# Optimization experiments

Hardware: AMD Instinct MI355X
Metric: run time of the kernel (lower is better)

## Reference

```python
import jax, jax.numpy as jnp
import numpy as np

B, C, H, W = 8, 4, 64, 2048
KH, KW = 3, 5
PH, PW = KH // 2, KW // 2
NUM_ITERS = 3
THETA_GAMMA = 0.9
THETA_ALPHA = 0.9
THETA_BETA = 0.015


def smoothness_kernel(theta):
    # Gaussian over squared window offsets, center zeroed, placed on class diagonal
    hs = jnp.arange(KH, dtype=jnp.float32) - KH // 2
    ws = jnp.arange(KW, dtype=jnp.float32) - KW // 2
    pdist = hs[:, None] ** 2 + ws[None, :] ** 2  # (KH,KW)
    k = jnp.exp(-pdist / (2.0 * theta ** 2))
    k = k.at[KH // 2, KW // 2].set(0.0)
    kernel = jnp.zeros((C, C, KH, KW), jnp.float32)
    kernel = kernel.at[jnp.arange(C), jnp.arange(C)].set(k)
    return kernel


def unfold_neighbors(x):
    # x: (b, c, H, W) -> (b, c, KH*KW-1, H*W), center tap excluded; row-major (kh,kw)
    b, c = x.shape[0], x.shape[1]
    xp = jnp.pad(x, ((0, 0), (0, 0), (PH, PH), (PW, PW)))
    taps = [xp[:, :, dh:dh + H, dw:dw + W]
            for dh in range(KH) for dw in range(KW)]
    K = KH * KW
    del taps[K // 2]  # exclude center pixel
    patches = jnp.stack(taps, axis=2)  # (b, c, K-1, H, W)
    return patches.reshape(b, c, K - 1, H * W)


def conv_same(x, kernel):
    return jax.lax.conv_general_dilated(
        x, kernel, window_strides=(1, 1), padding=[(PH, PH), (PW, PW)],
        dimension_numbers=('NCHW', 'OIHW', 'NCHW'))


def setup_inputs() -> dict:
    key = jax.random.key(0)
    k1, k2, k3 = jax.random.split(key, 3)
    unary = jax.random.normal(k1, (B, C, H, W), jnp.float32)
    xyz = jax.random.normal(k2, (B, 3, H, W), jnp.float32)
    mask = (jax.random.uniform(k3, (B, H, W)) > 0.1).astype(jnp.float32)
    weight_appearance = jnp.ones((1, C, 1, 1), jnp.float32) * 0.1
    weight_smoothness = jnp.ones((1, C, 1, 1), jnp.float32) * 0.02
    compat_w = 1.0 - jnp.eye(C, dtype=jnp.float32)  # Potts label compatibility (O,I)
    return {
        'unary': unary, 'xyz': xyz, 'mask': mask,
        'weight_appearance': weight_appearance,
        'weight_smoothness': weight_smoothness,
        'compat_w': compat_w,
    }


def reference(unary, xyz, mask, weight_appearance, weight_smoothness, compat_w):
    kernel_gamma = smoothness_kernel(THETA_GAMMA)
    kernel_alpha = smoothness_kernel(THETA_ALPHA)
    theta_beta = jnp.full((C,), THETA_BETA, jnp.float32)

    # precompute appearance (bilateral) kernel from xyz; detached in the original
    anchor = xyz.reshape(B, 3, 1, H * W)
    nb = unfold_neighbors(xyz)  # (B,3,14,HW)
    pdist = ((nb - anchor) ** 2).sum(axis=1, keepdims=True)  # (B,1,14,HW)
    kernel_beta = jnp.exp(-pdist / (2.0 * theta_beta[None, :, None, None] ** 2))  # (B,C,14,HW)
    kernel_beta = jax.lax.stop_gradient(kernel_beta)

    m = mask[:, None]  # (B,1,H,W)
    Q = unary
    for _ in range(NUM_ITERS):
        Q = jax.nn.softmax(Q, axis=1)
        k_smooth = conv_same(Q, kernel_gamma)
        # appearance message passing: masked windowed gather weighted by kernel_beta
        masked_Q = Q * m
        Q_nb = unfold_neighbors(masked_Q)  # (B,C,14,HW)
        exp_app = (Q_nb * kernel_beta).sum(axis=2).reshape(B, C, H, W) * m
        exp_smooth = conv_same(Q, kernel_alpha)
        k_app = exp_app * exp_smooth
        weighted_k = weight_smoothness * k_smooth + weight_appearance * k_app
        pairwise = jnp.einsum('oc,bchw->bohw', compat_w, weighted_k)
        Q = unary - pairwise
    return Q
```

## Files before the change

kernel.cpp:

```cpp
#include <hip/hip_runtime.h>
#include <hip/hip_fp16.h>

#define Bsz 8
#define Cn  4
#define Hn  64
#define Wn  2048
#define HW  (Hn*Wn)
#define NPIX (Bsz*HW)

#define PW     2052
#define PROWS  66
#define PBATCH (PW*PROWS)
#define PTOT   (Bsz*PBATCH)

#define G1 0.53940824f
#define G2 0.29096127f
#define G4 0.08465836f
#define G5 0.04566536f

struct Half4 { __half2 lo, hi; };
struct Half8 { __half2 h[4]; };

__device__ __forceinline__ __half2 bcast_lo(__half2 v) { return __half2half2(__low2half(v)); }
__device__ __forceinline__ __half2 bcast_hi(__half2 v) { return __half2half2(__high2half(v)); }

__global__ __launch_bounds__(256) void crf_prep(const float* __restrict__ unary,
                                                const float* __restrict__ xyz,
                                                const float* __restrict__ mask,
                                                Half8* __restrict__ BA,
                                                Half8* __restrict__ BB,
                                                Half4* __restrict__ S0,
                                                Half4* __restrict__ S1) {
    int c = blockIdx.x * 256 + threadIdx.x;
    if (c >= PTOT) return;
    int b  = c / PBATCH;
    int rr = c - b * PBATCH;
    int r  = rr / PW;
    int w  = rr - r * PW;
    int hp = r - 1, wp = w - 2;

    Half4 z; z.lo = __float2half2_rn(0.f); z.hi = z.lo;
    if (hp < 0 || hp >= Hn || wp < 0 || wp >= Wn) {
        S0[c] = z; S1[c] = z;
        return;
    }

    const size_t pl = (size_t)hp * Wn + wp;
    const size_t qb = (size_t)b * Cn * HW;
    const size_t xb = (size_t)b * 3 * HW;
    const size_t mb = (size_t)b * HW;

    float q0 = unary[qb + pl], q1 = unary[qb + pl + HW];
    float q2 = unary[qb + pl + 2 * HW], q3 = unary[qb + pl + 3 * HW];
    float mx = fmaxf(fmaxf(q0, q1), fmaxf(q2, q3));
    float e0 = __expf(q0 - mx), e1 = __expf(q1 - mx);
    float e2 = __expf(q2 - mx), e3 = __expf(q3 - mx);
    float inv = 1.0f / (e0 + e1 + e2 + e3);
    Half4 s; s.lo = __floats2half2_rn(e0 * inv, e1 * inv);
    s.hi = __floats2half2_rn(e2 * inv, e3 * inv);
    S0[c] = s;

    const float xcx = xyz[xb + pl], xcy = xyz[xb + pl + HW], xcz = xyz[xb + pl + 2 * HW];
    float bm[14];
    int t = 0;
#pragma unroll
    for (int dh = -1; dh <= 1; ++dh) {
#pragma unroll
        for (int dw = -2; dw <= 2; ++dw) {
            if (dh == 0 && dw == 0) continue;
            int hn = min(max(hp + dh, 0), Hn - 1);
            int wn = min(max(wp + dw, 0), Wn - 1);
            size_t pn = (size_t)hn * Wn + wn;
            float dx = xyz[xb + pn] - xcx;
            float dy = xyz[xb + pn + HW] - xcy;
            float dz = xyz[xb + pn + 2 * HW] - xcz;
            bm[t++] = __expf(-2222.2222f * (dx * dx + dy * dy + dz * dz)) * mask[mb + pn];
        }
    }
    Half8 a, bv;
    a.h[0] = __floats2half2_rn(bm[0], bm[1]);
    a.h[1] = __floats2half2_rn(bm[2], bm[3]);
    a.h[2] = __floats2half2_rn(bm[4], bm[5]);
    a.h[3] = __floats2half2_rn(bm[6], bm[7]);
    bv.h[0] = __floats2half2_rn(bm[8], bm[9]);
    bv.h[1] = __floats2half2_rn(bm[10], bm[11]);
    bv.h[2] = __floats2half2_rn(bm[12], bm[13]);
    bv.h[3] = __floats2half2_rn(mask[mb + pl], 0.f);
    const size_t pp = mb + pl;
    BA[pp] = a;
    BB[pp] = bv;
}

template<bool FINAL>
__global__ __launch_bounds__(256) void crf_pass(const Half4* __restrict__ Sin,
                                                Half4* __restrict__ Sout,
                                                const Half8* __restrict__ BA,
                                                const Half8* __restrict__ BB,
                                                const float* __restrict__ unary,
                                                const float* __restrict__ wa,
                                                const float* __restrict__ wsm,
                                                const float* __restrict__ cw,
                                                float* __restrict__ outp) {
    const int t = blockIdx.x * 256 + threadIdx.x;
    const int b  = t >> 17;
    const int hw = t & (HW - 1);
    const int h  = hw >> 11;
    const int w  = hw & (Wn - 1);
    const int cc = b * PBATCH + (h + 1) * PW + (w + 2);

    const Half8 ba = BA[t];
    const Half8 bb = BB[t];

    Half4 s0  = Sin[cc - PW - 2], s1  = Sin[cc - PW - 1], s2  = Sin[cc - PW];
    Half4 s3  = Sin[cc - PW + 1], s4  = Sin[cc - PW + 2];
    Half4 s5  = Sin[cc - 2],      s6  = Sin[cc - 1];
    Half4 s7  = Sin[cc + 1],      s8  = Sin[cc + 2];
    Half4 s9  = Sin[cc + PW - 2], s10 = Sin[cc + PW - 1], s11 = Sin[cc + PW];
    Half4 s12 = Sin[cc + PW + 1], s13 = Sin[cc + PW + 2];

    __half2 kl = __float2half2_rn(0.f), kh = kl, al = kl, ah = kl;

#define TAP(SV, GF, B2) do { \
        const __half2 g2_ = __float2half2_rn(GF); \
        kl = __hfma2(g2_, SV.lo, kl);  kh = __hfma2(g2_, SV.hi, kh); \
        const __half2 b2_ = (B2); \
        al = __hfma2(b2_, SV.lo, al);  ah = __hfma2(b2_, SV.hi, ah); \
    } while (0)

    TAP(s0,  G5, bcast_lo(ba.h[0]));  TAP(s1,  G2, bcast_hi(ba.h[0]));
    TAP(s2,  G1, bcast_lo(ba.h[1]));  TAP(s3,  G2, bcast_hi(ba.h[1]));
    TAP(s4,  G5, bcast_lo(ba.h[2]));
    TAP(s5,  G4, bcast_hi(ba.h[2]));  TAP(s6,  G1, bcast_lo(ba.h[3]));
    TAP(s7,  G1, bcast_hi(ba.h[3]));  TAP(s8,  G4, bcast_lo(bb.h[0]));
    TAP(s9,  G5, bcast_hi(bb.h[0]));  TAP(s10, G2, bcast_lo(bb.h[1]));
    TAP(s11, G1, bcast_hi(bb.h[1]));  TAP(s12, G2, bcast_lo(bb.h[2]));
    TAP(s13, G5, bcast_hi(bb.h[2]));
#undef TAP

    const float ksm[4] = {__low2float(kl), __high2float(kl), __low2float(kh), __high2float(kh)};
    const float app[4] = {__low2float(al), __high2float(al), __low2float(ah), __high2float(ah)};
    const float mc = __half2float(__low2half(bb.h[3]));

    float wk[4];
#pragma unroll
    for (int c = 0; c < 4; ++c)
        wk[c] = ksm[c] * (wsm[c] + wa[c] * (app[c] * mc));

    const size_t qb = (size_t)b * Cn * HW + hw;
    float q[4];
#pragma unroll
    for (int o = 0; o < 4; ++o) {
        float pw = cw[o*4+0]*wk[0] + cw[o*4+1]*wk[1] + cw[o*4+2]*wk[2] + cw[o*4+3]*wk[3];
        q[o] = unary[qb + (size_t)o * HW] - pw;
    }

    if (FINAL) {
#pragma unroll
        for (int o = 0; o < 4; ++o)
            outp[qb + (size_t)o * HW] = q[o];
    } else {
        float mx = fmaxf(fmaxf(q[0], q[1]), fmaxf(q[2], q[3]));
        float e0 = __expf(q[0] - mx), e1 = __expf(q[1] - mx);
        float e2 = __expf(q[2] - mx), e3 = __expf(q[3] - mx);
        float inv = 1.0f / (e0 + e1 + e2 + e3);
        Half4 s; s.lo = __floats2half2_rn(e0 * inv, e1 * inv);
        s.hi = __floats2half2_rn(e2 * inv, e3 * inv);
        Sout[cc] = s;
    }
}

extern "C" void kernel_launch(void* const* d_in, const int* in_sizes, int n_in,
                              void* d_out, int out_size, void* d_ws, size_t ws_size,
                              hipStream_t stream) {
    const float* unary  = (const float*)d_in[0];
    const float* xyz    = (const float*)d_in[1];
    const float* mask   = (const float*)d_in[2];
    const float* wa     = (const float*)d_in[3];
    const float* wsm    = (const float*)d_in[4];
    const float* compat = (const float*)d_in[5];
    float* outp = (float*)d_out;

    char* ws = (char*)d_ws;
    Half8* BA = (Half8*)ws;
    Half8* BB = (Half8*)(ws + (size_t)NPIX * 16);
    Half4* S0 = (Half4*)(ws + (size_t)NPIX * 32);
    Half4* S1 = (Half4*)(ws + (size_t)NPIX * 32 + (size_t)PTOT * 8);

    dim3 blk(256);
    crf_prep<<<dim3((PTOT + 255) / 256), blk, 0, stream>>>(unary, xyz, mask, BA, BB, S0, S1);
    crf_pass<false><<<dim3(NPIX / 256), blk, 0, stream>>>(S0, S1, BA, BB, unary, wa, wsm, compat, nullptr);
    crf_pass<false><<<dim3(NPIX / 256), blk, 0, stream>>>(S1, S0, BA, BB, unary, wa, wsm, compat, nullptr);
    crf_pass<true ><<<dim3(NPIX / 256), blk, 0, stream>>>(S0, nullptr, BA, BB, unary, wa, wsm, compat, outp);
}
```

Measured before the change: 127.5 us.

## Tile prep kernel through shared memory and compute two rows per pass thread

The prep kernel now stages a 6x68 halo tile of xyz and mask in shared memory as float4, so the 14 neighbour reads come from LDS instead of repeated global gathers. The pass kernel has each thread handle two vertically adjacent pixels and share the four loaded stencil rows, cutting redundant state loads. Padding borders are zeroed with a memset instead of inside the prep kernel. The cost is more registers per thread and half as many threads in the pass kernels, which may lower occupancy and latency hiding.

```diff
diff --git a/kernel.cpp b/kernel.cpp
--- a/kernel.cpp
+++ b/kernel.cpp
@@ -24,31 +24,82 @@
 __device__ __forceinline__ __half2 bcast_lo(__half2 v) { return __half2half2(__low2half(v)); }
 __device__ __forceinline__ __half2 bcast_hi(__half2 v) { return __half2half2(__high2half(v)); }
 
+__device__ __forceinline__ float Gw(int r, int d) {
+    const float Gt[3][5] = {{G5,G2,G1,G2,G5},{G4,G1,0.f,G1,G4},{G5,G2,G1,G2,G5}};
+    return Gt[r][d];
+}
+__device__ __forceinline__ constexpr int tap_of(int r, int d) {
+    return (r == 0) ? d : (r == 1) ? ((d < 2) ? 5 + d : 4 + d) : 9 + d;
+}
+__device__ __forceinline__ __half2 tapsel(const Half8& a, const Half8& bv, int t) {
+    __half2 h = (t < 8) ? a.h[t >> 1] : bv.h[(t - 8) >> 1];
+    return (t & 1) ? bcast_hi(h) : bcast_lo(h);
+}
+
 __global__ __launch_bounds__(256) void crf_prep(const float* __restrict__ unary,
                                                 const float* __restrict__ xyz,
                                                 const float* __restrict__ mask,
                                                 Half8* __restrict__ BA,
                                                 Half8* __restrict__ BB,
-                                                Half4* __restrict__ S0,
-                                                Half4* __restrict__ S1) {
-    int c = blockIdx.x * 256 + threadIdx.x;
-    if (c >= PTOT) return;
-    int b  = c / PBATCH;
-    int rr = c - b * PBATCH;
-    int r  = rr / PW;
-    int w  = rr - r * PW;
-    int hp = r - 1, wp = w - 2;
-
-    Half4 z; z.lo = __float2half2_rn(0.f); z.hi = z.lo;
-    if (hp < 0 || hp >= Hn || wp < 0 || wp >= Wn) {
-        S0[c] = z; S1[c] = z;
-        return;
-    }
-
-    const size_t pl = (size_t)hp * Wn + wp;
+                                                Half4* __restrict__ S0) {
+    __shared__ float4 XM[6 * 68];
+
+    const int tid = threadIdx.x;
+    const int w0 = blockIdx.x * 64;
+    const int h0 = blockIdx.y * 4;
+    const int b  = blockIdx.z;
+
     const size_t qb = (size_t)b * Cn * HW;
     const size_t xb = (size_t)b * 3 * HW;
     const size_t mb = (size_t)b * HW;
+
+#pragma unroll
+    for (int k = 0; k < 2; ++k) {
+        int i = tid + k * 256;
+        if (i < 6 * 68) {
+            int hr = i / 68, hc = i - hr * 68;
+            int gh = h0 + hr - 1, gw = w0 + hc - 2;
+            float4 xm = make_float4(0.f, 0.f, 0.f, 0.f);
+            if (gh >= 0 && gh < Hn && gw >= 0 && gw < Wn) {
+                size_t p = (size_t)gh * Wn + gw;
+                xm = make_float4(xyz[xb + p], xyz[xb + p + HW],
+                                 xyz[xb + p + 2 * HW], mask[mb + p]);
+            }
+            XM[i] = xm;
+        }
+    }
+    __syncthreads();
+
+    const int lw = tid & 63;
+    const int lr = tid >> 6;
+    const int li = (lr + 1) * 68 + (lw + 2);
+    const int hp = h0 + lr, wp = w0 + lw;
+    const size_t pl = (size_t)hp * Wn + wp;
+
+    const float4 xc = XM[li];
+    float bm[14];
+    int t = 0;
+#pragma unroll
+    for (int dh = -1; dh <= 1; ++dh) {
+#pragma unroll
+        for (int dw = -2; dw <= 2; ++dw) {
+            if (dh == 0 && dw == 0) continue;
+            float4 xn = XM[li + dh * 68 + dw];
+            float dx = xn.x - xc.x, dy = xn.y - xc.y, dz = xn.z - xc.z;
+            bm[t++] = __expf(-2222.2222f * (dx * dx + dy * dy + dz * dz)) * xn.w;
+        }
+    }
+    Half8 a, bv;
+    a.h[0]  = __floats2half2_rn(bm[0],  bm[1]);
+    a.h[1]  = __floats2half2_rn(bm[2],  bm[3]);
+    a.h[2]  = __floats2half2_rn(bm[4],  bm[5]);
+    a.h[3]  = __floats2half2_rn(bm[6],  bm[7]);
+    bv.h[0] = __floats2half2_rn(bm[8],  bm[9]);
+    bv.h[1] = __floats2half2_rn(bm[10], bm[11]);
+    bv.h[2] = __floats2half2_rn(bm[12], bm[13]);
+    bv.h[3] = __floats2half2_rn(xc.w, 0.f);
+    BA[mb + pl] = a;
+    BB[mb + pl] = bv;
 
     float q0 = unary[qb + pl], q1 = unary[qb + pl + HW];
     float q2 = unary[qb + pl + 2 * HW], q3 = unary[qb + pl + 3 * HW];
@@ -58,37 +109,43 @@
     float inv = 1.0f / (e0 + e1 + e2 + e3);
     Half4 s; s.lo = __floats2half2_rn(e0 * inv, e1 * inv);
     s.hi = __floats2half2_rn(e2 * inv, e3 * inv);
-    S0[c] = s;
-
-    const float xcx = xyz[xb + pl], xcy = xyz[xb + pl + HW], xcz = xyz[xb + pl + 2 * HW];
-    float bm[14];
-    int t = 0;
-#pragma unroll
-    for (int dh = -1; dh <= 1; ++dh) {
-#pragma unroll
-        for (int dw = -2; dw <= 2; ++dw) {
-            if (dh == 0 && dw == 0) continue;
-            int hn = min(max(hp + dh, 0), Hn - 1);
-            int wn = min(max(wp + dw, 0), Wn - 1);
-            size_t pn = (size_t)hn * Wn + wn;
-            float dx = xyz[xb + pn] - xcx;
-            float dy = xyz[xb + pn + HW] - xcy;
-            float dz = xyz[xb + pn + 2 * HW] - xcz;
-            bm[t++] = __expf(-2222.2222f * (dx * dx + dy * dy + dz * dz)) * mask[mb + pn];
-        }
-    }
-    Half8 a, bv;
-    a.h[0] = __floats2half2_rn(bm[0], bm[1]);
-    a.h[1] = __floats2half2_rn(bm[2], bm[3]);
-    a.h[2] = __floats2half2_rn(bm[4], bm[5]);
-    a.h[3] = __floats2half2_rn(bm[6], bm[7]);
-    bv.h[0] = __floats2half2_rn(bm[8], bm[9]);
-    bv.h[1] = __floats2half2_rn(bm[10], bm[11]);
-    bv.h[2] = __floats2half2_rn(bm[12], bm[13]);
-    bv.h[3] = __floats2half2_rn(mask[mb + pl], 0.f);
-    const size_t pp = mb + pl;
-    BA[pp] = a;
-    BB[pp] = bv;
+    S0[b * PBATCH + (hp + 1) * PW + (wp + 2)] = s;
+}
+
+template<bool FINAL>
+__device__ __forceinline__ void finish_px(__half2 kl, __half2 kh, __half2 al, __half2 ah,
+                                          float mc, size_t qb, int cc,
+                                          const float* __restrict__ unary,
+                                          const float* __restrict__ wa,
+                                          const float* __restrict__ wsm,
+                                          const float* __restrict__ cw,
+                                          float* __restrict__ outp,
+                                          Half4* __restrict__ Sout) {
+    const float ksm[4] = {__low2float(kl), __high2float(kl), __low2float(kh), __high2float(kh)};
+    const float app[4] = {__low2float(al), __high2float(al), __low2float(ah), __high2float(ah)};
+    float wk[4];
+#pragma unroll
+    for (int c = 0; c < 4; ++c)
+        wk[c] = ksm[c] * (wsm[c] + wa[c] * (app[c] * mc));
+    float q[4];
+#pragma unroll
+    for (int o = 0; o < 4; ++o) {
+        float pw = cw[o*4+0]*wk[0] + cw[o*4+1]*wk[1] + cw[o*4+2]*wk[2] + cw[o*4+3]*wk[3];
+        q[o] = unary[qb + (size_t)o * HW] - pw;
+    }
+    if (FINAL) {
+#pragma unroll
+        for (int o = 0; o < 4; ++o)
+            outp[qb + (size_t)o * HW] = q[o];
+    } else {
+        float mx = fmaxf(fmaxf(q[0], q[1]), fmaxf(q[2], q[3]));
+        float e0 = __expf(q[0] - mx), e1 = __expf(q[1] - mx);
+        float e2 = __expf(q[2] - mx), e3 = __expf(q[3] - mx);
+        float inv = 1.0f / (e0 + e1 + e2 + e3);
+        Half4 s; s.lo = __floats2half2_rn(e0 * inv, e1 * inv);
+        s.hi = __floats2half2_rn(e2 * inv, e3 * inv);
+        Sout[cc] = s;
+    }
 }
 
 template<bool FINAL>
@@ -101,72 +158,58 @@
                                                 const float* __restrict__ wsm,
                                                 const float* __restrict__ cw,
                                                 float* __restrict__ outp) {
-    const int t = blockIdx.x * 256 + threadIdx.x;
-    const int b  = t >> 17;
-    const int hw = t & (HW - 1);
-    const int h  = hw >> 11;
-    const int w  = hw & (Wn - 1);
-    const int cc = b * PBATCH + (h + 1) * PW + (w + 2);
-
-    const Half8 ba = BA[t];
-    const Half8 bb = BB[t];
-
-    Half4 s0  = Sin[cc - PW - 2], s1  = Sin[cc - PW - 1], s2  = Sin[cc - PW];
-    Half4 s3  = Sin[cc - PW + 1], s4  = Sin[cc - PW + 2];
-    Half4 s5  = Sin[cc - 2],      s6  = Sin[cc - 1];
-    Half4 s7  = Sin[cc + 1],      s8  = Sin[cc + 2];
-    Half4 s9  = Sin[cc + PW - 2], s10 = Sin[cc + PW - 1], s11 = Sin[cc + PW];
-    Half4 s12 = Sin[cc + PW + 1], s13 = Sin[cc + PW + 2];
-
-    __half2 kl = __float2half2_rn(0.f), kh = kl, al = kl, ah = kl;
-
-#define TAP(SV, GF, B2) do { \
-        const __half2 g2_ = __float2half2_rn(GF); \
-        kl = __hfma2(g2_, SV.lo, kl);  kh = __hfma2(g2_, SV.hi, kh); \
-        const __half2 b2_ = (B2); \
-        al = __hfma2(b2_, SV.lo, al);  ah = __hfma2(b2_, SV.hi, ah); \
-    } while (0)
-
-    TAP(s0,  G5, bcast_lo(ba.h[0]));  TAP(s1,  G2, bcast_hi(ba.h[0]));
-    TAP(s2,  G1, bcast_lo(ba.h[1]));  TAP(s3,  G2, bcast_hi(ba.h[1]));
-    TAP(s4,  G5, bcast_lo(ba.h[2]));
-    TAP(s5,  G4, bcast_hi(ba.h[2]));  TAP(s6,  G1, bcast_lo(ba.h[3]));
-    TAP(s7,  G1, bcast_hi(ba.h[3]));  TAP(s8,  G4, bcast_lo(bb.h[0]));
-    TAP(s9,  G5, bcast_hi(bb.h[0]));  TAP(s10, G2, bcast_lo(bb.h[1]));
-    TAP(s11, G1, bcast_hi(bb.h[1]));  TAP(s12, G2, bcast_lo(bb.h[2]));
-    TAP(s13, G5, bcast_hi(bb.h[2]));
-#undef TAP
-
-    const float ksm[4] = {__low2float(kl), __high2float(kl), __low2float(kh), __high2float(kh)};
-    const float app[4] = {__low2float(al), __high2float(al), __low2float(ah), __high2float(ah)};
-    const float mc = __half2float(__low2half(bb.h[3]));
-
-    float wk[4];
-#pragma unroll
-    for (int c = 0; c < 4; ++c)
-        wk[c] = ksm[c] * (wsm[c] + wa[c] * (app[c] * mc));
-
-    const size_t qb = (size_t)b * Cn * HW + hw;
-    float q[4];
-#pragma unroll
-    for (int o = 0; o < 4; ++o) {
-        float pw = cw[o*4+0]*wk[0] + cw[o*4+1]*wk[1] + cw[o*4+2]*wk[2] + cw[o*4+3]*wk[3];
-        q[o] = unary[qb + (size_t)o * HW] - pw;
-    }
-
-    if (FINAL) {
-#pragma unroll
-        for (int o = 0; o < 4; ++o)
-            outp[qb + (size_t)o * HW] = q[o];
-    } else {
-        float mx = fmaxf(fmaxf(q[0], q[1]), fmaxf(q[2], q[3]));
-        float e0 = __expf(q[0] - mx), e1 = __expf(q[1] - mx);
-        float e2 = __expf(q[2] - mx), e3 = __expf(q[3] - mx);
-        float inv = 1.0f / (e0 + e1 + e2 + e3);
-        Half4 s; s.lo = __floats2half2_rn(e0 * inv, e1 * inv);
-        s.hi = __floats2half2_rn(e2 * inv, e3 * inv);
-        Sout[cc] = s;
-    }
+    const int t  = blockIdx.x * 256 + threadIdx.x;
+    const int b  = t >> 16;
+    const int r2 = t & 65535;
+    const int ph = r2 >> 11;
+    const int w  = r2 & (Wn - 1);
+    const int h0p = 2 * ph;
+
+    const size_t t0 = (size_t)b * HW + (size_t)h0p * Wn + w;
+    const int cc0 = b * PBATCH + (h0p + 1) * PW + (w + 2);
+
+    const Half8 ba0 = BA[t0],      bb0 = BB[t0];
+    const Half8 ba1 = BA[t0 + Wn], bb1 = BB[t0 + Wn];
+
+    Half4 s[4][5];
+#pragma unroll
+    for (int r = 0; r < 4; ++r) {
+        const int base = cc0 + (r - 1) * PW;
+#pragma unroll
+        for (int d = 0; d < 5; ++d) s[r][d] = Sin[base + d - 2];
+    }
+
+    const __half2 z2 = __float2half2_rn(0.f);
+    __half2 k0l=z2,k0h=z2,a0l=z2,a0h=z2, k1l=z2,k1h=z2,a1l=z2,a1h=z2;
+
+#pragma unroll
+    for (int r = 0; r < 4; ++r) {
+#pragma unroll
+        for (int d = 0; d < 5; ++d) {
+            if (r <= 2 && !(r == 1 && d == 2)) {
+                const __half2 g2 = __float2half2_rn(Gw(r, d));
+                k0l = __hfma2(g2, s[r][d].lo, k0l);
+                k0h = __hfma2(g2, s[r][d].hi, k0h);
+                const __half2 b2 = tapsel(ba0, bb0, tap_of(r, d));
+                a0l = __hfma2(b2, s[r][d].lo, a0l);
+                a0h = __hfma2(b2, s[r][d].hi, a0h);
+            }
+            if (r >= 1 && !(r == 2 && d == 2)) {
+                const __half2 g2 = __float2half2_rn(Gw(r - 1, d));
+                k1l = __hfma2(g2, s[r][d].lo, k1l);
+                k1h = __hfma2(g2, s[r][d].hi, k1h);
+                const __half2 b2 = tapsel(ba1, bb1, tap_of(r - 1, d));
+                a1l = __hfma2(b2, s[r][d].lo, a1l);
+                a1h = __hfma2(b2, s[r][d].hi, a1h);
+            }
+        }
+    }
+
+    const size_t qb0 = (size_t)b * Cn * HW + (size_t)h0p * Wn + w;
+    finish_px<FINAL>(k0l, k0h, a0l, a0h, __half2float(__low2half(bb0.h[3])),
+                     qb0, cc0, unary, wa, wsm, cw, outp, Sout);
+    finish_px<FINAL>(k1l, k1h, a1l, a1h, __half2float(__low2half(bb1.h[3])),
+                     qb0 + Wn, cc0 + PW, unary, wa, wsm, cw, outp, Sout);
 }
 
 extern "C" void kernel_launch(void* const* d_in, const int* in_sizes, int n_in,
@@ -186,9 +229,12 @@
     Half4* S0 = (Half4*)(ws + (size_t)NPIX * 32);
     Half4* S1 = (Half4*)(ws + (size_t)NPIX * 32 + (size_t)PTOT * 8);
 
+    hipMemsetAsync(S0, 0, (size_t)PTOT * 8 * 2, stream);
+
     dim3 blk(256);
-    crf_prep<<<dim3((PTOT + 255) / 256), blk, 0, stream>>>(unary, xyz, mask, BA, BB, S0, S1);
-    crf_pass<false><<<dim3(NPIX / 256), blk, 0, stream>>>(S0, S1, BA, BB, unary, wa, wsm, compat, nullptr);
-    crf_pass<false><<<dim3(NPIX / 256), blk, 0, stream>>>(S1, S0, BA, BB, unary, wa, wsm, compat, nullptr);
-    crf_pass<true ><<<dim3(NPIX / 256), blk, 0, stream>>>(S0, nullptr, BA, BB, unary, wa, wsm, compat, outp);
-}
+    crf_prep<<<dim3(Wn / 64, Hn / 4, Bsz), blk, 0, stream>>>(unary, xyz, mask, BA, BB, S0);
+    dim3 pgrid(NPIX / 2 / 256);
+    crf_pass<false><<<pgrid, blk, 0, stream>>>(S0, S1, BA, BB, unary, wa, wsm, compat, nullptr);
+    crf_pass<false><<<pgrid, blk, 0, stream>>>(S1, S0, BA, BB, unary, wa, wsm, compat, nullptr);
+    crf_pass<true ><<<pgrid, blk, 0, stream>>>(S0, nullptr, BA, BB, unary, wa, wsm, compat, outp);
+}
```

Result: slower. 135.1 us (+5.9%).
